# Optimization experiments

Measured on AMD Instinct MI355X. Metric: run time of the kernel, lower is better.

## Reference

```python
import jax, jax.numpy as jnp
import numpy as np

INPUT_DIM = 512
HIDDEN_DIM = 256
REP_DIM = 256
SCORE_HIDDEN = 128


def setup_inputs() -> dict:
    key = jax.random.key(0)
    ks = jax.random.split(key, 12)
    def rn(k, shape, scale=None):
        s = scale if scale is not None else 1.0 / np.sqrt(shape[0])
        return jax.random.normal(k, shape, dtype=jnp.float32) * s
    return {
        "feat_x": jax.random.normal(ks[0], (512, INPUT_DIM), dtype=jnp.float32),
        "feat_pos": jax.random.normal(ks[1], (512, INPUT_DIM), dtype=jnp.float32),
        "feat_neg": jax.random.normal(ks[2], (512, INPUT_DIM), dtype=jnp.float32),
        # g: Linear(input,hidden) -> GELU -> Linear(hidden,rep); stored as x @ W
        "g_w1": rn(ks[3], (INPUT_DIM, HIDDEN_DIM)),
        "g_b1": jnp.zeros((HIDDEN_DIM,), jnp.float32),
        "g_w2": rn(ks[4], (HIDDEN_DIM, REP_DIM)),
        "g_b2": jnp.zeros((REP_DIM,), jnp.float32),
        # out_proj: Linear(rep, input, bias=False)
        "out_w": rn(ks[5], (REP_DIM, INPUT_DIM)),
        # score_net: Linear(3*rep+1, score_hidden) -> GELU -> Linear(score_hidden, 1)
        "s_w1": rn(ks[6], (3 * REP_DIM + 1, SCORE_HIDDEN)),
        "s_b1": jnp.zeros((SCORE_HIDDEN,), jnp.float32),
        "s_w2": rn(ks[7], (SCORE_HIDDEN, 1)),
        "s_b2": jnp.zeros((1,), jnp.float32),
    }


def _gelu(x):
    return jax.nn.gelu(x, approximate=False)  # torch nn.GELU default = exact erf


def _g(x, g_w1, g_b1, g_w2, g_b2):
    return _gelu(x @ g_w1 + g_b1) @ g_w2 + g_b2


def _set_operator(feat_x, feat_set, params):
    g_w1, g_b1, g_w2, g_b2, out_w, s_w1, s_b1, s_w2, s_b2 = params
    x_rep = _g(feat_x, g_w1, g_b1, g_w2, g_b2)   # (n, r)
    y_rep = _g(feat_set, g_w1, g_b1, g_w2, g_b2)  # (m, r)
    n, r = x_rep.shape
    m = y_rep.shape[0]
    x_exp = jnp.broadcast_to(x_rep[:, None, :], (n, m, r))
    y_exp = jnp.broadcast_to(y_rep[None, :, :], (n, m, r))
    delta = y_exp - x_exp                                   # (n, m, r)
    delta_norm = jnp.linalg.norm(delta, axis=-1, keepdims=True)
    score_in = jnp.concatenate([x_exp, y_exp, delta, delta_norm], axis=-1)  # (n, m, 3r+1)
    logits = (_gelu(score_in @ s_w1 + s_b1) @ s_w2 + s_b2)[..., 0]          # (n, m)
    weights = jax.nn.softmax(logits, axis=1)
    set_update_rep = jnp.einsum("nm,nmr->nr", weights, delta)
    return set_update_rep @ out_w


def reference(feat_x, feat_pos, feat_neg, g_w1, g_b1, g_w2, g_b2, out_w, s_w1, s_b1, s_w2, s_b2):
    params = (g_w1, g_b1, g_w2, g_b2, out_w, s_w1, s_b1, s_w2, s_b2)
    s_pos = _set_operator(feat_x, feat_pos, params)
    s_neg = _set_operator(feat_x, feat_neg, params)  # mask_self_neg=False
    return s_pos - s_neg
```

## Files before the change

### kernel.cpp

```cpp
#include <hip/hip_runtime.h>
#include <math.h>

#define NN 512
#define IN 512
#define HD 256
#define RD 256
#define SH 128

__device__ __forceinline__ float gelu_fast(float x){
    const float z  = x * 0.70710678118654752f;
    const float az = fabsf(z);
    const float t  = __builtin_amdgcn_rcpf(fmaf(0.3275911f, az, 1.0f));
    float p = fmaf(1.061405429f, t, -1.453152027f);
    p = fmaf(p, t, 1.421413741f);
    p = fmaf(p, t, -0.284496736f);
    p = fmaf(p, t, 0.254829592f);
    p = p * t;
    const float e = __builtin_amdgcn_exp2f(z * z * -1.4426950408889634f);
    const float E = p * e;
    const float one_plus_erf = (x >= 0.0f) ? (2.0f - E) : E;
    return 0.5f * x * one_plus_erf;
}

__global__ __launch_bounds__(512) void k_rep(
    const float* __restrict__ fx, const float* __restrict__ fp, const float* __restrict__ fn,
    const float* __restrict__ w1, const float* __restrict__ b1,
    const float* __restrict__ w2, const float* __restrict__ b2,
    const float* __restrict__ s_w1,
    float* __restrict__ r_x, float* __restrict__ r_p, float* __restrict__ r_n,
    float* __restrict__ r_pT, float* __restrict__ r_nT,
    float* __restrict__ A_x, float* __restrict__ BT_p, float* __restrict__ BT_n)
{
    __shared__ float xs[4][IN];
    __shared__ float ps[8][4][HD];
    __shared__ float hs[4][HD];
    __shared__ float rloc[4][RD];
    __shared__ float ab4[4][SH];
    const int t = threadIdx.x;
    const int mat = blockIdx.x >> 7;
    const int row0 = (blockIdx.x & 127) << 2;
    const float* src = (mat==0) ? fx : (mat==1) ? fp : fn;

    {
        const int j = t >> 7, c4 = (t & 127) << 2;
        *(float4*)&xs[j][c4] = *(const float4*)&src[(row0+j)*IN + c4];
    }
    __syncthreads();

    const int cg = t & 63, s = t >> 6;
    const int c0 = cg << 2;

    {
        float4 acc[4];
        #pragma unroll
        for (int j=0;j<4;j++) acc[j] = make_float4(0.f,0.f,0.f,0.f);
        const float* wp = w1 + (s*64)*HD + c0;
        #pragma unroll 8
        for (int ii=0; ii<64; ii++){
            float4 w = *(const float4*)wp; wp += HD;
            const int i = s*64 + ii;
            #pragma unroll
            for (int j=0;j<4;j++){
                const float xv = xs[j][i];
                acc[j].x = fmaf(xv, w.x, acc[j].x);
                acc[j].y = fmaf(xv, w.y, acc[j].y);
                acc[j].z = fmaf(xv, w.z, acc[j].z);
                acc[j].w = fmaf(xv, w.w, acc[j].w);
            }
        }
        #pragma unroll
        for (int j=0;j<4;j++) *(float4*)&ps[s][j][c0] = acc[j];
    }
    __syncthreads();

    #pragma unroll
    for (int rep=0; rep<2; rep++){
        const int idx = rep*512 + t;
        const int j = idx >> 8, c = idx & 255;
        float v = b1[c];
        #pragma unroll
        for (int ss=0; ss<8; ss++) v += ps[ss][j][c];
        hs[j][c] = gelu_fast(v);
    }
    __syncthreads();

    {
        float4 acc[4];
        #pragma unroll
        for (int j=0;j<4;j++) acc[j] = make_float4(0.f,0.f,0.f,0.f);
        const float* wp = w2 + (s*32)*RD + c0;
        #pragma unroll 8
        for (int ii=0; ii<32; ii++){
            float4 w = *(const float4*)wp; wp += RD;
            const int i = s*32 + ii;
            #pragma unroll
            for (int j=0;j<4;j++){
                const float xv = hs[j][i];
                acc[j].x = fmaf(xv, w.x, acc[j].x);
                acc[j].y = fmaf(xv, w.y, acc[j].y);
                acc[j].z = fmaf(xv, w.z, acc[j].z);
                acc[j].w = fmaf(xv, w.w, acc[j].w);
            }
        }
        #pragma unroll
        for (int j=0;j<4;j++) *(float4*)&ps[s][j][c0] = acc[j];
    }
    __syncthreads();

    float* rout = (mat==0) ? r_x : (mat==1) ? r_p : r_n;
    #pragma unroll
    for (int rep=0; rep<2; rep++){
        const int idx = rep*512 + t;
        const int j = idx >> 8, c = idx & 255;
        float v = b2[c];
        #pragma unroll
        for (int ss=0; ss<8; ss++) v += ps[ss][j][c];
        rloc[j][c] = v;
        rout[(row0+j)*RD + c] = v;
    }
    __syncthreads();

    if (mat && t < 256){
        float* rT = (mat==1) ? r_pT : r_nT;
        float4 q = make_float4(rloc[0][t], rloc[1][t], rloc[2][t], rloc[3][t]);
        *(float4*)&rT[t*NN + row0] = q;
    }

    {
        const int cg2 = t & 31, s2 = t >> 5;
        const int cc0 = cg2 << 2;
        const float sgn = (mat==0) ? -1.0f : 1.0f;
        const int base1 = (mat==0) ? 0 : 256;
        const float* p1 = s_w1 + (base1 + s2*16)*SH + cc0;
        const float* p3 = s_w1 + (512   + s2*16)*SH + cc0;
        float4 a[4];
        #pragma unroll
        for (int j=0;j<4;j++) a[j] = make_float4(0.f,0.f,0.f,0.f);
        #pragma unroll 8
        for (int ii=0; ii<16; ii++){
            float4 wa = *(const float4*)p1; p1 += SH;
            float4 wd = *(const float4*)p3; p3 += SH;
            float4 w;
            w.x = fmaf(sgn, wd.x, wa.x);
            w.y = fmaf(sgn, wd.y, wa.y);
            w.z = fmaf(sgn, wd.z, wa.z);
            w.w = fmaf(sgn, wd.w, wa.w);
            const int i = s2*16 + ii;
            #pragma unroll
            for (int j=0;j<4;j++){
                const float xv = rloc[j][i];
                a[j].x = fmaf(xv, w.x, a[j].x);
                a[j].y = fmaf(xv, w.y, a[j].y);
                a[j].z = fmaf(xv, w.z, a[j].z);
                a[j].w = fmaf(xv, w.w, a[j].w);
            }
        }
        float* psf = &ps[0][0][0];
        #pragma unroll
        for (int j=0;j<4;j++) *(float4*)&psf[(s2*4 + j)*SH + cc0] = a[j];
    }
    __syncthreads();

    {
        const float* psf = &ps[0][0][0];
        const int j = t >> 7, c = t & 127;
        float v = 0.f;
        #pragma unroll
        for (int ss=0; ss<16; ss++) v += psf[(ss*4 + j)*SH + c];
        if (mat==0) A_x[(row0+j)*SH + c] = v;
        else        ab4[j][c] = v;
    }
    __syncthreads();
    if (mat && t < 128){
        float* BT = (mat==1) ? BT_p : BT_n;
        float4 q = make_float4(ab4[0][t], ab4[1][t], ab4[2][t], ab4[3][t]);
        *(float4*)&BT[t*NN + row0] = q;
    }
}

__global__ __launch_bounds__(256) void k_sd(
    const float* __restrict__ r_x, const float* __restrict__ r_pT, const float* __restrict__ r_nT,
    const float* __restrict__ A_x, const float* __restrict__ BT_p, const float* __restrict__ BT_n,
    const float* __restrict__ s_w1, const float* __restrict__ s_b1,
    const float* __restrict__ s_w2,
    float* __restrict__ E_p, float* __restrict__ E_n, float* __restrict__ Spart)
{
    __shared__ float xs[2][RD];
    __shared__ float cw2[SH][2];
    __shared__ float2 wz2[SH];
    __shared__ float nxv[2];
    __shared__ float ssum[2][2];
    const int t = threadIdx.x;
    const int set = blockIdx.x >> 10;
    const int rem = blockIdx.x & 1023;
    const int n0 = (rem >> 2) << 1;
    const int mt = rem & 3;
    const int mbase = mt << 7;
    const int tm = t & 127, tn = t >> 7;
    const int m = mbase + tm;
    const float* yT = set ? r_nT : r_pT;
    const float* BT = set ? BT_n : BT_p;
    float* E = set ? E_n : E_p;

    xs[0][t] = r_x[n0*RD + t];
    xs[1][t] = r_x[(n0+1)*RD + t];
    if (t < SH){
        cw2[t][0] = A_x[n0*SH + t] + s_b1[t];
        cw2[t][1] = A_x[(n0+1)*SH + t] + s_b1[t];
        wz2[t] = make_float2(s_w1[768*SH + t], 0.5f*s_w2[t]);
    }
    __syncthreads();
    {
        const int w = t >> 6, lane = t & 63;
        if (w < 2){
            float v = 0.f;
            #pragma unroll
            for (int q=0;q<4;q++){ const float e = xs[w][lane + 64*q]; v = fmaf(e,e,v); }
            #pragma unroll
            for (int off=32; off>=1; off>>=1) v += __shfl_xor(v, off);
            if (lane==0) nxv[w] = v;
        }
    }
    __syncthreads();

    float d = 0.f, ny = 0.f;
    {
        const float* yp = yT + m;
        #pragma unroll 8
        for (int r=0; r<RD; r++){
            const float y = *yp; yp += NN;
            d  = fmaf(xs[tn][r], y, d);
            ny = fmaf(y, y, ny);
        }
    }
    const float dn = sqrtf(fmaxf(fmaf(-2.f, d, nxv[tn] + ny), 0.f));

    float acc = 0.f;
    {
        const float* bp = BT + m;
        #pragma unroll 4
        for (int k=0; k<SH; k++){
            const float b = *bp; bp += NN;
            const float cw = cw2[k][tn];
            const float2 wz = wz2[k];
            const float u = fmaf(dn, wz.x, cw + b);
            const float z  = u * 0.70710678118654752f;
            const float az = fabsf(z);
            const float tt = __builtin_amdgcn_rcpf(fmaf(0.3275911f, az, 1.0f));
            float p = fmaf(1.061405429f, tt, -1.453152027f);
            p = fmaf(p, tt, 1.421413741f);
            p = fmaf(p, tt, -0.284496736f);
            p = fmaf(p, tt, 0.254829592f);
            p = p * tt;
            const float e2 = __builtin_amdgcn_exp2f(z * z * -1.4426950408889634f);
            const float Eq = p * e2;
            const float ope = (u >= 0.0f) ? (2.0f - Eq) : Eq;
            acc = fmaf(wz.y, u * ope, acc);
        }
    }
    const float ev = __builtin_amdgcn_exp2f(acc * 1.4426950408889634f);
    E[(n0+tn)*NN + m] = ev;

    float v = ev;
    #pragma unroll
    for (int off=32; off>=1; off>>=1) v += __shfl_xor(v, off);
    if ((t & 63) == 0) ssum[tn][(t >> 6) & 1] = v;
    __syncthreads();
    if (t < 2) Spart[(set*4 + mt)*NN + n0 + t] = ssum[t][0] + ssum[t][1];
}

__global__ __launch_bounds__(256) void k_dv(
    const float* __restrict__ E_p, const float* __restrict__ E_n,
    const float* __restrict__ Spart,
    const float* __restrict__ r_p, const float* __restrict__ r_n,
    float* __restrict__ psum)
{
    __shared__ float rinv[8];
    __shared__ float wbuf[2][64][4];
    const int t = threadIdx.x;
    const int nt = blockIdx.x >> 3;
    const int ms = blockIdx.x & 7;
    const int n0 = nt << 2, mbase = ms << 6;

    if (t < 8){
        const int se = t >> 2, n = n0 + (t & 3);
        float S = 0.f;
        #pragma unroll
        for (int q=0;q<4;q++) S += Spart[(se*4+q)*NN + n];
        rinv[t] = 1.0f / S;
    }
    __syncthreads();
    #pragma unroll
    for (int rep=0; rep<2; rep++){
        const int idx = rep*256 + t;
        const int se = idx >> 8, j = (idx >> 6) & 3, mm = idx & 63;
        const float* E = se ? E_n : E_p;
        wbuf[se][mm][j] = E[(n0+j)*NN + mbase + mm] * rinv[se*4 + j];
    }
    __syncthreads();

    float acc[4] = {0.f,0.f,0.f,0.f};
    {
        const float* rp = r_p + mbase*RD + t;
        #pragma unroll 4
        for (int mm=0; mm<64; mm++){
            const float rv = *rp; rp += RD;
            const float4 wa = *(const float4*)&wbuf[0][mm][0];
            acc[0]=fmaf(wa.x,rv,acc[0]); acc[1]=fmaf(wa.y,rv,acc[1]);
            acc[2]=fmaf(wa.z,rv,acc[2]); acc[3]=fmaf(wa.w,rv,acc[3]);
        }
    }
    {
        const float* rn = r_n + mbase*RD + t;
        #pragma unroll 4
        for (int mm=0; mm<64; mm++){
            const float rv = -(*rn); rn += RD;
            const float4 wa = *(const float4*)&wbuf[1][mm][0];
            acc[0]=fmaf(wa.x,rv,acc[0]); acc[1]=fmaf(wa.y,rv,acc[1]);
            acc[2]=fmaf(wa.z,rv,acc[2]); acc[3]=fmaf(wa.w,rv,acc[3]);
        }
    }
    float* P = psum + ms*(NN*RD);
    #pragma unroll
    for (int j=0;j<4;j++) P[(n0+j)*RD + t] = acc[j];
}

__global__ __launch_bounds__(256) void k_out(
    const float* __restrict__ psum, const float* __restrict__ out_w,
    float* __restrict__ out)
{
    __shared__ float dv2[2][RD];
    __shared__ float ps[2][2][128];
    const int t = threadIdx.x;
    const int nt = blockIdx.x >> 2;
    const int cb = (blockIdx.x & 3) << 7;
    const int n0 = nt << 1;

    #pragma unroll
    for (int j=0;j<2;j++){
        float v = 0.f;
        #pragma unroll
        for (int ms=0; ms<8; ms++) v += psum[ms*(NN*RD) + (n0+j)*RD + t];
        dv2[j][t] = v;
    }
    __syncthreads();

    const int cc = t & 127, s = t >> 7;
    float a0 = 0.f, a1 = 0.f;
    const float* wo = out_w + (s*128)*IN + cb + cc;
    #pragma unroll 4
    for (int rr=0; rr<128; rr++){
        const float w = *wo; wo += IN;
        a0 = fmaf(dv2[0][s*128 + rr], w, a0);
        a1 = fmaf(dv2[1][s*128 + rr], w, a1);
    }
    ps[s][0][cc] = a0;
    ps[s][1][cc] = a1;
    __syncthreads();
    {
        const int j = t >> 7, c = t & 127;
        out[(n0+j)*IN + cb + c] = ps[0][j][c] + ps[1][j][c];
    }
}

extern "C" void kernel_launch(void* const* d_in, const int* in_sizes, int n_in,
                              void* d_out, int out_size, void* d_ws, size_t ws_size,
                              hipStream_t stream)
{
    const float* fx  = (const float*)d_in[0];
    const float* fp  = (const float*)d_in[1];
    const float* fn  = (const float*)d_in[2];
    const float* gw1 = (const float*)d_in[3];
    const float* gb1 = (const float*)d_in[4];
    const float* gw2 = (const float*)d_in[5];
    const float* gb2 = (const float*)d_in[6];
    const float* ow  = (const float*)d_in[7];
    const float* sw1 = (const float*)d_in[8];
    const float* sb1 = (const float*)d_in[9];
    const float* sw2 = (const float*)d_in[10];
    float* out = (float*)d_out;

    float* ws   = (float*)d_ws;
    float* r_x  = ws;
    float* r_p  = r_x  + 131072;
    float* r_n  = r_p  + 131072;
    float* r_pT = r_n  + 131072;
    float* r_nT = r_pT + 131072;
    float* A_x  = r_nT + 131072;
    float* BT_p = A_x  + 65536;
    float* BT_n = BT_p + 65536;
    float* E_p  = BT_n + 65536;
    float* E_n  = E_p  + 262144;
    float* Spar = E_n  + 262144;
    float* psum = Spar + 4096;

    hipLaunchKernelGGL(k_rep, dim3(384), dim3(512), 0, stream,
                       fx, fp, fn, gw1, gb1, gw2, gb2, sw1,
                       r_x, r_p, r_n, r_pT, r_nT, A_x, BT_p, BT_n);
    hipLaunchKernelGGL(k_sd, dim3(2048), dim3(256), 0, stream,
                       r_x, r_pT, r_nT, A_x, BT_p, BT_n,
                       sw1, sb1, sw2, E_p, E_n, Spar);
    hipLaunchKernelGGL(k_dv, dim3(1024), dim3(256), 0, stream,
                       E_p, E_n, Spar, r_p, r_n, psum);
    hipLaunchKernelGGL(k_out, dim3(1024), dim3(256), 0, stream,
                       psum, ow, out);
}
```

Baseline: 175.6 us.

## Drop transposed rep buffers and split score work by K-halves per thread

k_rep now runs 768 blocks of 256 threads on 2 rows each and writes row-major B and rep outputs, so the transposed copies r_pT/r_nT/BT are gone. k_sd now reads y and B rows contiguously with float4 loads. Each thread handles both n rows over half of the reduction dimension, and the two halves are combined through shared memory. GELU constants are folded so the score loop does less work per element. The goal is to cut strided global loads and the transpose scatter writes, at the cost of extra shared-memory exchanges and syncs.

```diff
diff --git a/kernel.cpp b/kernel.cpp
--- a/kernel.cpp
+++ b/kernel.cpp
@@ -22,28 +22,41 @@
     return 0.5f * x * one_plus_erf;
 }
 
-__global__ __launch_bounds__(512) void k_rep(
+__device__ __forceinline__ float gelu2(float u){
+    const float az = fabsf(u);
+    const float tt = __builtin_amdgcn_rcpf(fmaf(0.23166045f, az, 1.0f));
+    float p = fmaf(1.061405429f, tt, -1.453152027f);
+    p = fmaf(p, tt, 1.421413741f);
+    p = fmaf(p, tt, -0.284496736f);
+    p = fmaf(p, tt, 0.254829592f);
+    p = p * tt;
+    const float e2 = __builtin_amdgcn_exp2f(u * u * -0.72134752044448170f);
+    const float Eq = p * e2;
+    const float ope = (u >= 0.0f) ? (2.0f - Eq) : Eq;
+    return u * ope;
+}
+
+__global__ __launch_bounds__(256) void k_rep(
     const float* __restrict__ fx, const float* __restrict__ fp, const float* __restrict__ fn,
     const float* __restrict__ w1, const float* __restrict__ b1,
     const float* __restrict__ w2, const float* __restrict__ b2,
     const float* __restrict__ s_w1,
     float* __restrict__ r_x, float* __restrict__ r_p, float* __restrict__ r_n,
-    float* __restrict__ r_pT, float* __restrict__ r_nT,
-    float* __restrict__ A_x, float* __restrict__ BT_p, float* __restrict__ BT_n)
+    float* __restrict__ A_x, float* __restrict__ B_p, float* __restrict__ B_n)
 {
-    __shared__ float xs[4][IN];
-    __shared__ float ps[8][4][HD];
-    __shared__ float hs[4][HD];
-    __shared__ float rloc[4][RD];
-    __shared__ float ab4[4][SH];
+    __shared__ float xs[2][IN];
+    __shared__ float ps[4][2][HD];
+    __shared__ float hs[2][HD];
+    __shared__ float rloc[2][RD];
+    __shared__ float psf[8][2][SH];
     const int t = threadIdx.x;
-    const int mat = blockIdx.x >> 7;
-    const int row0 = (blockIdx.x & 127) << 2;
+    const int mat = blockIdx.x >> 8;
+    const int row0 = (blockIdx.x & 255) << 1;
     const float* src = (mat==0) ? fx : (mat==1) ? fp : fn;
 
     {
-        const int j = t >> 7, c4 = (t & 127) << 2;
-        *(float4*)&xs[j][c4] = *(const float4*)&src[(row0+j)*IN + c4];
+        const int j = t >> 7, q = (t & 127) << 2;
+        *(float4*)&xs[j][q] = *(const float4*)&src[(row0+j)*IN + q];
     }
     __syncthreads();
 
@@ -51,93 +64,71 @@
     const int c0 = cg << 2;
 
     {
-        float4 acc[4];
-        #pragma unroll
-        for (int j=0;j<4;j++) acc[j] = make_float4(0.f,0.f,0.f,0.f);
-        const float* wp = w1 + (s*64)*HD + c0;
+        float4 a0 = make_float4(0.f,0.f,0.f,0.f), a1 = a0;
+        const float* wp = w1 + (s*128)*HD + c0;
+        #pragma unroll 8
+        for (int ii=0; ii<128; ii++){
+            float4 w = *(const float4*)wp; wp += HD;
+            const int i = s*128 + ii;
+            const float x0 = xs[0][i], x1 = xs[1][i];
+            a0.x = fmaf(x0, w.x, a0.x); a0.y = fmaf(x0, w.y, a0.y);
+            a0.z = fmaf(x0, w.z, a0.z); a0.w = fmaf(x0, w.w, a0.w);
+            a1.x = fmaf(x1, w.x, a1.x); a1.y = fmaf(x1, w.y, a1.y);
+            a1.z = fmaf(x1, w.z, a1.z); a1.w = fmaf(x1, w.w, a1.w);
+        }
+        *(float4*)&ps[s][0][c0] = a0;
+        *(float4*)&ps[s][1][c0] = a1;
+    }
+    __syncthreads();
+
+    #pragma unroll
+    for (int rep=0; rep<2; rep++){
+        const int idx = rep*256 + t;
+        const int j = idx >> 8, c = idx & 255;
+        const float v = b1[c] + ps[0][j][c] + ps[1][j][c] + ps[2][j][c] + ps[3][j][c];
+        hs[j][c] = gelu_fast(v);
+    }
+    __syncthreads();
+
+    {
+        float4 a0 = make_float4(0.f,0.f,0.f,0.f), a1 = a0;
+        const float* wp = w2 + (s*64)*RD + c0;
         #pragma unroll 8
         for (int ii=0; ii<64; ii++){
-            float4 w = *(const float4*)wp; wp += HD;
+            float4 w = *(const float4*)wp; wp += RD;
             const int i = s*64 + ii;
-            #pragma unroll
-            for (int j=0;j<4;j++){
-                const float xv = xs[j][i];
-                acc[j].x = fmaf(xv, w.x, acc[j].x);
-                acc[j].y = fmaf(xv, w.y, acc[j].y);
-                acc[j].z = fmaf(xv, w.z, acc[j].z);
-                acc[j].w = fmaf(xv, w.w, acc[j].w);
-            }
-        }
-        #pragma unroll
-        for (int j=0;j<4;j++) *(float4*)&ps[s][j][c0] = acc[j];
-    }
-    __syncthreads();
-
-    #pragma unroll
-    for (int rep=0; rep<2; rep++){
-        const int idx = rep*512 + t;
-        const int j = idx >> 8, c = idx & 255;
-        float v = b1[c];
-        #pragma unroll
-        for (int ss=0; ss<8; ss++) v += ps[ss][j][c];
-        hs[j][c] = gelu_fast(v);
-    }
-    __syncthreads();
-
-    {
-        float4 acc[4];
-        #pragma unroll
-        for (int j=0;j<4;j++) acc[j] = make_float4(0.f,0.f,0.f,0.f);
-        const float* wp = w2 + (s*32)*RD + c0;
-        #pragma unroll 8
-        for (int ii=0; ii<32; ii++){
-            float4 w = *(const float4*)wp; wp += RD;
-            const int i = s*32 + ii;
-            #pragma unroll
-            for (int j=0;j<4;j++){
-                const float xv = hs[j][i];
-                acc[j].x = fmaf(xv, w.x, acc[j].x);
-                acc[j].y = fmaf(xv, w.y, acc[j].y);
-                acc[j].z = fmaf(xv, w.z, acc[j].z);
-                acc[j].w = fmaf(xv, w.w, acc[j].w);
-            }
-        }
-        #pragma unroll
-        for (int j=0;j<4;j++) *(float4*)&ps[s][j][c0] = acc[j];
+            const float x0 = hs[0][i], x1 = hs[1][i];
+            a0.x = fmaf(x0, w.x, a0.x); a0.y = fmaf(x0, w.y, a0.y);
+            a0.z = fmaf(x0, w.z, a0.z); a0.w = fmaf(x0, w.w, a0.w);
+            a1.x = fmaf(x1, w.x, a1.x); a1.y = fmaf(x1, w.y, a1.y);
+            a1.z = fmaf(x1, w.z, a1.z); a1.w = fmaf(x1, w.w, a1.w);
+        }
+        *(float4*)&ps[s][0][c0] = a0;
+        *(float4*)&ps[s][1][c0] = a1;
     }
     __syncthreads();
 
     float* rout = (mat==0) ? r_x : (mat==1) ? r_p : r_n;
     #pragma unroll
     for (int rep=0; rep<2; rep++){
-        const int idx = rep*512 + t;
+        const int idx = rep*256 + t;
         const int j = idx >> 8, c = idx & 255;
-        float v = b2[c];
-        #pragma unroll
-        for (int ss=0; ss<8; ss++) v += ps[ss][j][c];
+        const float v = b2[c] + ps[0][j][c] + ps[1][j][c] + ps[2][j][c] + ps[3][j][c];
         rloc[j][c] = v;
         rout[(row0+j)*RD + c] = v;
     }
     __syncthreads();
-
-    if (mat && t < 256){
-        float* rT = (mat==1) ? r_pT : r_nT;
-        float4 q = make_float4(rloc[0][t], rloc[1][t], rloc[2][t], rloc[3][t]);
-        *(float4*)&rT[t*NN + row0] = q;
-    }
 
     {
         const int cg2 = t & 31, s2 = t >> 5;
         const int cc0 = cg2 << 2;
         const float sgn = (mat==0) ? -1.0f : 1.0f;
         const int base1 = (mat==0) ? 0 : 256;
-        const float* p1 = s_w1 + (base1 + s2*16)*SH + cc0;
-        const float* p3 = s_w1 + (512   + s2*16)*SH + cc0;
-        float4 a[4];
-        #pragma unroll
-        for (int j=0;j<4;j++) a[j] = make_float4(0.f,0.f,0.f,0.f);
+        const float* p1 = s_w1 + (base1 + s2*32)*SH + cc0;
+        const float* p3 = s_w1 + (512   + s2*32)*SH + cc0;
+        float4 a0 = make_float4(0.f,0.f,0.f,0.f), a1 = a0;
         #pragma unroll 8
-        for (int ii=0; ii<16; ii++){
+        for (int ii=0; ii<32; ii++){
             float4 wa = *(const float4*)p1; p1 += SH;
             float4 wd = *(const float4*)p3; p3 += SH;
             float4 w;
@@ -145,128 +136,133 @@
             w.y = fmaf(sgn, wd.y, wa.y);
             w.z = fmaf(sgn, wd.z, wa.z);
             w.w = fmaf(sgn, wd.w, wa.w);
-            const int i = s2*16 + ii;
-            #pragma unroll
-            for (int j=0;j<4;j++){
-                const float xv = rloc[j][i];
-                a[j].x = fmaf(xv, w.x, a[j].x);
-                a[j].y = fmaf(xv, w.y, a[j].y);
-                a[j].z = fmaf(xv, w.z, a[j].z);
-                a[j].w = fmaf(xv, w.w, a[j].w);
-            }
-        }
-        float* psf = &ps[0][0][0];
-        #pragma unroll
-        for (int j=0;j<4;j++) *(float4*)&psf[(s2*4 + j)*SH + cc0] = a[j];
-    }
-    __syncthreads();
-
-    {
-        const float* psf = &ps[0][0][0];
+            const int i = s2*32 + ii;
+            const float x0 = rloc[0][i], x1 = rloc[1][i];
+            a0.x = fmaf(x0, w.x, a0.x); a0.y = fmaf(x0, w.y, a0.y);
+            a0.z = fmaf(x0, w.z, a0.z); a0.w = fmaf(x0, w.w, a0.w);
+            a1.x = fmaf(x1, w.x, a1.x); a1.y = fmaf(x1, w.y, a1.y);
+            a1.z = fmaf(x1, w.z, a1.z); a1.w = fmaf(x1, w.w, a1.w);
+        }
+        *(float4*)&psf[s2][0][cc0] = a0;
+        *(float4*)&psf[s2][1][cc0] = a1;
+    }
+    __syncthreads();
+
+    {
         const int j = t >> 7, c = t & 127;
         float v = 0.f;
         #pragma unroll
-        for (int ss=0; ss<16; ss++) v += psf[(ss*4 + j)*SH + c];
-        if (mat==0) A_x[(row0+j)*SH + c] = v;
-        else        ab4[j][c] = v;
-    }
-    __syncthreads();
-    if (mat && t < 128){
-        float* BT = (mat==1) ? BT_p : BT_n;
-        float4 q = make_float4(ab4[0][t], ab4[1][t], ab4[2][t], ab4[3][t]);
-        *(float4*)&BT[t*NN + row0] = q;
+        for (int ss=0; ss<8; ss++) v += psf[ss][j][c];
+        float* dst = (mat==0) ? A_x : (mat==1) ? B_p : B_n;
+        dst[(row0+j)*SH + c] = v;
     }
 }
 
 __global__ __launch_bounds__(256) void k_sd(
-    const float* __restrict__ r_x, const float* __restrict__ r_pT, const float* __restrict__ r_nT,
-    const float* __restrict__ A_x, const float* __restrict__ BT_p, const float* __restrict__ BT_n,
+    const float* __restrict__ r_x, const float* __restrict__ r_p, const float* __restrict__ r_n,
+    const float* __restrict__ A_x, const float* __restrict__ B_p, const float* __restrict__ B_n,
     const float* __restrict__ s_w1, const float* __restrict__ s_b1,
     const float* __restrict__ s_w2,
     float* __restrict__ E_p, float* __restrict__ E_n, float* __restrict__ Spart)
 {
-    __shared__ float xs[2][RD];
-    __shared__ float cw2[SH][2];
-    __shared__ float2 wz2[SH];
-    __shared__ float nxv[2];
-    __shared__ float ssum[2][2];
+    __shared__ float4 xs4[2][64];
+    __shared__ float4 cmb[SH];
+    __shared__ float4 pd[128][2];
+    __shared__ float nx[2];
+    __shared__ float ssum[4];
     const int t = threadIdx.x;
     const int set = blockIdx.x >> 10;
     const int rem = blockIdx.x & 1023;
     const int n0 = (rem >> 2) << 1;
     const int mt = rem & 3;
     const int mbase = mt << 7;
-    const int tm = t & 127, tn = t >> 7;
+    const int tm = t & 127, kh = t >> 7;
     const int m = mbase + tm;
-    const float* yT = set ? r_nT : r_pT;
-    const float* BT = set ? BT_n : BT_p;
+    const float* ry = set ? r_n : r_p;
+    const float* B  = set ? B_n : B_p;
     float* E = set ? E_n : E_p;
 
-    xs[0][t] = r_x[n0*RD + t];
-    xs[1][t] = r_x[(n0+1)*RD + t];
-    if (t < SH){
-        cw2[t][0] = A_x[n0*SH + t] + s_b1[t];
-        cw2[t][1] = A_x[(n0+1)*SH + t] + s_b1[t];
-        wz2[t] = make_float2(s_w1[768*SH + t], 0.5f*s_w2[t]);
-    }
-    __syncthreads();
-    {
-        const int w = t >> 6, lane = t & 63;
-        if (w < 2){
-            float v = 0.f;
+    if (t < 128){
+        const int j = t >> 6, q = t & 63;
+        xs4[j][q] = *(const float4*)&r_x[(n0+j)*RD + (q << 2)];
+    } else {
+        const int k = t - 128;
+        cmb[k] = make_float4(A_x[n0*SH + k] + s_b1[k],
+                             A_x[(n0+1)*SH + k] + s_b1[k],
+                             s_w1[768*SH + k],
+                             0.5f * s_w2[k]);
+    }
+    __syncthreads();
+
+    if (t < 128){
+        const int row = t >> 6, lane = t & 63;
+        const float4 q = xs4[row][lane];
+        float v = q.x*q.x + q.y*q.y + q.z*q.z + q.w*q.w;
+        #pragma unroll
+        for (int off=32; off>=1; off>>=1) v += __shfl_xor(v, off);
+        if (lane==0) nx[row] = v;
+    }
+
+    float d0=0.f, d1=0.f, ny=0.f;
+    {
+        const float* yp = ry + m*RD + (kh << 7);
+        #pragma unroll
+        for (int q=0; q<32; q++){
+            const float4 y = *(const float4*)(yp + (q << 2));
+            const float4 x0 = xs4[0][(kh << 5) + q];
+            const float4 x1 = xs4[1][(kh << 5) + q];
+            d0 = fmaf(x0.x,y.x,d0); d0 = fmaf(x0.y,y.y,d0);
+            d0 = fmaf(x0.z,y.z,d0); d0 = fmaf(x0.w,y.w,d0);
+            d1 = fmaf(x1.x,y.x,d1); d1 = fmaf(x1.y,y.y,d1);
+            d1 = fmaf(x1.z,y.z,d1); d1 = fmaf(x1.w,y.w,d1);
+            ny = fmaf(y.x,y.x,ny); ny = fmaf(y.y,y.y,ny);
+            ny = fmaf(y.z,y.z,ny); ny = fmaf(y.w,y.w,ny);
+        }
+    }
+    pd[tm][kh] = make_float4(d0, d1, ny, 0.f);
+    __syncthreads();
+    {
+        const float4 o = pd[tm][1-kh];
+        d0 += o.x; d1 += o.y; ny += o.z;
+    }
+    const float dn0 = sqrtf(fmaxf(fmaf(-2.f, d0, nx[0] + ny), 0.f));
+    const float dn1 = sqrtf(fmaxf(fmaf(-2.f, d1, nx[1] + ny), 0.f));
+
+    float acc0 = 0.f, acc1 = 0.f;
+    {
+        const float* bp = B + m*SH + (kh << 6);
+        #pragma unroll 4
+        for (int q=0; q<16; q++){
+            const float4 b4 = *(const float4*)(bp + (q << 2));
+            const float bb[4] = {b4.x, b4.y, b4.z, b4.w};
             #pragma unroll
-            for (int q=0;q<4;q++){ const float e = xs[w][lane + 64*q]; v = fmaf(e,e,v); }
-            #pragma unroll
-            for (int off=32; off>=1; off>>=1) v += __shfl_xor(v, off);
-            if (lane==0) nxv[w] = v;
-        }
-    }
-    __syncthreads();
-
-    float d = 0.f, ny = 0.f;
-    {
-        const float* yp = yT + m;
-        #pragma unroll 8
-        for (int r=0; r<RD; r++){
-            const float y = *yp; yp += NN;
-            d  = fmaf(xs[tn][r], y, d);
-            ny = fmaf(y, y, ny);
-        }
-    }
-    const float dn = sqrtf(fmaxf(fmaf(-2.f, d, nxv[tn] + ny), 0.f));
-
-    float acc = 0.f;
-    {
-        const float* bp = BT + m;
-        #pragma unroll 4
-        for (int k=0; k<SH; k++){
-            const float b = *bp; bp += NN;
-            const float cw = cw2[k][tn];
-            const float2 wz = wz2[k];
-            const float u = fmaf(dn, wz.x, cw + b);
-            const float z  = u * 0.70710678118654752f;
-            const float az = fabsf(z);
-            const float tt = __builtin_amdgcn_rcpf(fmaf(0.3275911f, az, 1.0f));
-            float p = fmaf(1.061405429f, tt, -1.453152027f);
-            p = fmaf(p, tt, 1.421413741f);
-            p = fmaf(p, tt, -0.284496736f);
-            p = fmaf(p, tt, 0.254829592f);
-            p = p * tt;
-            const float e2 = __builtin_amdgcn_exp2f(z * z * -1.4426950408889634f);
-            const float Eq = p * e2;
-            const float ope = (u >= 0.0f) ? (2.0f - Eq) : Eq;
-            acc = fmaf(wz.y, u * ope, acc);
-        }
-    }
-    const float ev = __builtin_amdgcn_exp2f(acc * 1.4426950408889634f);
-    E[(n0+tn)*NN + m] = ev;
-
-    float v = ev;
-    #pragma unroll
-    for (int off=32; off>=1; off>>=1) v += __shfl_xor(v, off);
-    if ((t & 63) == 0) ssum[tn][(t >> 6) & 1] = v;
-    __syncthreads();
-    if (t < 2) Spart[(set*4 + mt)*NN + n0 + t] = ssum[t][0] + ssum[t][1];
+            for (int kk=0; kk<4; kk++){
+                const float4 c = cmb[(kh << 6) + (q << 2) + kk];
+                const float u0 = fmaf(dn0, c.z, c.x + bb[kk]);
+                const float u1 = fmaf(dn1, c.z, c.y + bb[kk]);
+                acc0 = fmaf(c.w, gelu2(u0), acc0);
+                acc1 = fmaf(c.w, gelu2(u1), acc1);
+            }
+        }
+    }
+    __syncthreads();
+    pd[tm][kh] = make_float4(acc0, acc1, 0.f, 0.f);
+    __syncthreads();
+    {
+        const float4 o = pd[tm][1-kh];
+        const float tot = (kh==0) ? (acc0 + o.x) : (acc1 + o.y);
+        const float ev = __builtin_amdgcn_exp2f(tot * 1.4426950408889634f);
+        E[(n0+kh)*NN + m] = ev;
+        float v = ev;
+        #pragma unroll
+        for (int off=32; off>=1; off>>=1) v += __shfl_xor(v, off);
+        if ((t & 63) == 0) ssum[t >> 6] = v;
+    }
+    __syncthreads();
+    if (t == 0){
+        Spart[(set*4 + mt)*NN + n0]     = ssum[0] + ssum[1];
+        Spart[(set*4 + mt)*NN + n0 + 1] = ssum[2] + ssum[3];
+    }
 }
 
 __global__ __launch_bounds__(256) void k_dv(
@@ -384,21 +380,19 @@
     float* r_x  = ws;
     float* r_p  = r_x  + 131072;
     float* r_n  = r_p  + 131072;
-    float* r_pT = r_n  + 131072;
-    float* r_nT = r_pT + 131072;
-    float* A_x  = r_nT + 131072;
-    float* BT_p = A_x  + 65536;
-    float* BT_n = BT_p + 65536;
-    float* E_p  = BT_n + 65536;
+    float* A_x  = r_n  + 131072;
+    float* B_p  = A_x  + 65536;
+    float* B_n  = B_p  + 65536;
+    float* E_p  = B_n  + 65536;
     float* E_n  = E_p  + 262144;
     float* Spar = E_n  + 262144;
     float* psum = Spar + 4096;
 
-    hipLaunchKernelGGL(k_rep, dim3(384), dim3(512), 0, stream,
+    hipLaunchKernelGGL(k_rep, dim3(768), dim3(256), 0, stream,
                        fx, fp, fn, gw1, gb1, gw2, gb2, sw1,
-                       r_x, r_p, r_n, r_pT, r_nT, A_x, BT_p, BT_n);
+                       r_x, r_p, r_n, A_x, B_p, B_n);
     hipLaunchKernelGGL(k_sd, dim3(2048), dim3(256), 0, stream,
-                       r_x, r_pT, r_nT, A_x, BT_p, BT_n,
+                       r_x, r_p, r_n, A_x, B_p, B_n,
                        sw1, sb1, sw2, E_p, E_n, Spar);
     hipLaunchKernelGGL(k_dv, dim3(1024), dim3(256), 0, stream,
                        E_p, E_n, Spar, r_p, r_n, psum);
```

Result: slower. 183.4 us (+4.5%).
